# Performance work log

Measured on AMD Instinct MI355X. Metric: run time of the kernel, lower is better.

The kernel has to match this reference:

```python
import jax, jax.numpy as jnp
import numpy as np

HIDDEN = 1024
HEADS = 16
HEAD_DIM = HIDDEN // HEADS


def setup_inputs() -> dict:
    key = jax.random.key(0)
    ks = jax.random.split(key, 7)
    B, S, H = 8, 1024, HIDDEN
    hidden_states = jax.random.normal(ks[0], (B, S, H), dtype=jnp.float32)
    attention_mask = jnp.zeros((B, 1, 1, S), dtype=jnp.float32)
    # Xavier-uniform weights [out, in], zero biases (matches module init)
    limit = float(np.sqrt(6.0 / (H + H)))
    Wq = jax.random.uniform(ks[1], (H, H), minval=-limit, maxval=limit, dtype=jnp.float32)
    Wk = jax.random.uniform(ks[2], (H, H), minval=-limit, maxval=limit, dtype=jnp.float32)
    Wv = jax.random.uniform(ks[3], (H, H), minval=-limit, maxval=limit, dtype=jnp.float32)
    bq = jnp.zeros((H,), dtype=jnp.float32)
    bk = jnp.zeros((H,), dtype=jnp.float32)
    bv = jnp.zeros((H,), dtype=jnp.float32)
    return {"hidden_states": hidden_states, "attention_mask": attention_mask,
            "Wq": Wq, "bq": bq, "Wk": Wk, "bk": bk, "Wv": Wv, "bv": bv}


def _split_heads(x):
    # [B, S, H] -> [B, heads, S, head_dim]
    B, S, _ = x.shape
    return x.reshape(B, S, HEADS, HEAD_DIM).transpose(0, 2, 1, 3)


def reference(hidden_states, attention_mask, Wq, bq, Wk, bk, Wv, bv):
    # Linear projections: y = x @ W^T + b  (weights stored [out, in] as in torch)
    q = _split_heads(hidden_states @ Wq.T + bq)
    k = _split_heads(hidden_states @ Wk.T + bk)
    v = _split_heads(hidden_states @ Wv.T + bv)
    scale = 1.0 / (HEAD_DIM ** 0.5)
    scores = jnp.einsum('bhqd,bhkd->bhqk', q, k) * scale  # [B,heads,S,S]
    scores = scores + attention_mask
    probs = jax.nn.softmax(scores, axis=-1)
    # dropout is identity at inference
    ctx = jnp.einsum('bhqk,bhkd->bhqd', probs, v)
    B, _, S, _ = ctx.shape
    return ctx.transpose(0, 2, 1, 3).reshape(B, S, HIDDEN)
```

## Files before the change

kernel.cpp:

```cpp
#include <hip/hip_runtime.h>
#include <hip/hip_bf16.h>
#include <stdint.h>

#define B_ 8
#define S_ 1024
#define NH_ 16
#define D_ 64
#define H_ 1024
#define M_TOT (B_*S_)
#define LOG2E 1.44269504088896f

typedef __attribute__((ext_vector_type(8))) short short8;
typedef __attribute__((ext_vector_type(4))) float f32x4;
typedef __attribute__((ext_vector_type(16))) float f32x16;

#if __has_builtin(__builtin_amdgcn_exp2f)
#define EXP2(x) __builtin_amdgcn_exp2f(x)
#else
#define EXP2(x) __expf((x) * 0.69314718056f)
#endif

static __device__ __forceinline__ unsigned short f2bf(float f) {
  union { float f; unsigned u; } c; c.f = f;
  unsigned u = c.u;
  return (unsigned short)((u + 0x7fffu + ((u >> 16) & 1u)) >> 16);
}

static __device__ __forceinline__ void gld_lds16(void* lds, const void* g) {
  __builtin_amdgcn_global_load_lds((const __attribute__((address_space(1))) unsigned*)g,
                                   (__attribute__((address_space(3))) unsigned*)lds, 16, 0, 0);
}

#define WAIT_LGKM0() asm volatile("s_waitcnt lgkmcnt(0)" ::: "memory")
#define WAIT_VM(n)   asm volatile("s_waitcnt vmcnt(" #n ")" ::: "memory")
#define SBAR()       __builtin_amdgcn_s_barrier()
#define SCHED0()     __builtin_amdgcn_sched_barrier(0)

__global__ void cvt_f32_bf16(const float* __restrict__ X,
                             const float* __restrict__ Wq,
                             const float* __restrict__ Wk,
                             const float* __restrict__ Wv,
                             unsigned short* __restrict__ Xbf,
                             unsigned short* __restrict__ Wbf) {
  const long long NX = (long long)M_TOT * H_;
  const long long NW = (long long)H_ * H_;
  long long t = (long long)blockIdx.x * blockDim.x + threadIdx.x;
  const long long stride = (long long)gridDim.x * blockDim.x;
  const long long total4 = (NX + 3 * NW) >> 2;
  for (; t < total4; t += stride) {
    long long e = t << 2;
    const float* src; unsigned short* dst;
    if (e < NX) { src = X + e; dst = Xbf + e; }
    else {
      long long r = e - NX;
      int w = (int)(r / NW);
      long long o = r - (long long)w * NW;
      src = (w == 0 ? Wq : (w == 1 ? Wk : Wv)) + o;
      dst = Wbf + (long long)w * NW + o;
    }
    float4 v = *(const float4*)src;
    ushort4 u;
    u.x = f2bf(v.x); u.y = f2bf(v.y); u.z = f2bf(v.z); u.w = f2bf(v.w);
    *(ushort4*)dst = u;
  }
}

#define QBM 256
#define QBN 128
#define QBK 64
#define BUFSZ 49152

__global__ __launch_bounds__(512, 2) void qkv_gemm(
    const unsigned short* __restrict__ Xbf,
    const unsigned short* __restrict__ Wbf,
    const float* __restrict__ bq, const float* __restrict__ bk,
    const float* __restrict__ bv,
    unsigned short* __restrict__ Qo, unsigned short* __restrict__ Ko,
    unsigned short* __restrict__ Vt) {
  __shared__ char lds[3 * BUFSZ];

  const int tid = threadIdx.x;
  const int w = tid >> 6;
  const int l = tid & 63;
  const int lrow = l & 15, lgrp = l >> 4;
  const int wm = w >> 1, wn = w & 1;

  const int orig = blockIdx.x;
  const int id = (orig & 7) * 96 + (orig >> 3);
  const int mtile = (id & 31) * QBM;
  const int rest = id >> 5;
  const int ntile = (rest & 7) * QBN;
  const int z = rest >> 3;

  const unsigned short* Wz = Wbf + (long long)z * H_ * H_;

  const int srow = l >> 3;
  const int sslot = l & 7;
  auto stageA = [&](char* buf, int j, int k0) {
    int row = j * 8 + srow;
    int so = (sslot ^ (row & 7)) * 8;
    gld_lds16(buf + j * 1024, Xbf + (long long)(mtile + row) * H_ + k0 + so);
  };
  auto stageB = [&](char* buf, int j, int k0) {
    int row = j * 8 + srow;
    int so = (sslot ^ (row & 7)) * 8;
    gld_lds16(buf + 32768 + j * 1024, Wz + (long long)(ntile + row) * H_ + k0 + so);
  };

  const int strA = (z == 2 ? wn : wm) * 64;
  const int strB = (z == 2 ? wm : wn) * 64;
  const int offA = (z == 2) ? 32768 : 0;
  const int offB = (z == 2) ? 0 : 32768;
  auto rdA = [&](char* buf, int mh, int sub, int ks) -> short8 {
    int r = strA + mh * 32 + sub * 16 + lrow;
    return *(const short8*)(buf + offA + r * 128 + (((ks * 4 + lgrp) ^ (r & 7)) * 16));
  };
  auto rdB = [&](char* buf, int nh, int sub, int ks) -> short8 {
    int r = strB + nh * 32 + sub * 16 + lrow;
    return *(const short8*)(buf + offB + r * 128 + (((ks * 4 + lgrp) ^ (r & 7)) * 16));
  };

  f32x4 acc[4][4];
  f32x4 zero = {0.f, 0.f, 0.f, 0.f};
  #pragma unroll
  for (int i = 0; i < 4; ++i)
    #pragma unroll
    for (int j = 0; j < 4; ++j) acc[i][j] = zero;

  {
    char* b0p = lds;
    char* b1p = lds + BUFSZ;
    #pragma unroll
    for (int c = 0; c < 4; ++c) stageA(b0p, w * 4 + c, 0);
    stageB(b0p, w * 2 + 0, 0); stageB(b0p, w * 2 + 1, 0);
    #pragma unroll
    for (int c = 0; c < 4; ++c) stageA(b1p, w * 4 + c, QBK);
    stageB(b1p, w * 2 + 0, QBK); stageB(b1p, w * 2 + 1, QBK);
  }
  WAIT_VM(6);
  SBAR();

  #pragma unroll 1
  for (int t = 0; t < 16; ++t) {
    char* buf  = lds + (t % 3) * BUFSZ;
    char* nbuf = lds + ((t + 2) % 3) * BUFSZ;
    const int k0n = (t + 2) * QBK;
    const bool st = (t + 2 < 16);

    short8 af[2][2], b0[2][2], b1[2][2];

    #pragma unroll
    for (int sub = 0; sub < 2; ++sub)
      #pragma unroll
      for (int ks = 0; ks < 2; ++ks) {
        af[sub][ks] = rdA(buf, 0, sub, ks);
        b0[sub][ks] = rdB(buf, 0, sub, ks);
      }
    if (st) { stageA(nbuf, w * 4 + 0, k0n); stageA(nbuf, w * 4 + 1, k0n); }
    SBAR();
    WAIT_LGKM0(); SCHED0();
    __builtin_amdgcn_s_setprio(1);
    #pragma unroll
    for (int sa = 0; sa < 2; ++sa)
      #pragma unroll
      for (int sb = 0; sb < 2; ++sb)
        #pragma unroll
        for (int ks = 0; ks < 2; ++ks)
          acc[sa][sb] = __builtin_amdgcn_mfma_f32_16x16x32_bf16(
              af[sa][ks], b0[sb][ks], acc[sa][sb], 0, 0, 0);
    __builtin_amdgcn_s_setprio(0);
    SBAR();

    #pragma unroll
    for (int sub = 0; sub < 2; ++sub)
      #pragma unroll
      for (int ks = 0; ks < 2; ++ks)
        b1[sub][ks] = rdB(buf, 1, sub, ks);
    if (st) { stageA(nbuf, w * 4 + 2, k0n); stageA(nbuf, w * 4 + 3, k0n); }
    SBAR();
    WAIT_LGKM0(); SCHED0();
    __builtin_amdgcn_s_setprio(1);
    #pragma unroll
    for (int sa = 0; sa < 2; ++sa)
      #pragma unroll
      for (int sb = 0; sb < 2; ++sb)
        #pragma unroll
        for (int ks = 0; ks < 2; ++ks)
          acc[sa][2 + sb] = __builtin_amdgcn_mfma_f32_16x16x32_bf16(
              af[sa][ks], b1[sb][ks], acc[sa][2 + sb], 0, 0, 0);
    __builtin_amdgcn_s_setprio(0);
    SBAR();

    #pragma unroll
    for (int sub = 0; sub < 2; ++sub)
      #pragma unroll
      for (int ks = 0; ks < 2; ++ks)
        af[sub][ks] = rdA(buf, 1, sub, ks);
    if (st) { stageB(nbuf, w * 2 + 0, k0n); stageB(nbuf, w * 2 + 1, k0n); }
    SBAR();
    WAIT_LGKM0(); SCHED0();
    __builtin_amdgcn_s_setprio(1);
    #pragma unroll
    for (int sa = 0; sa < 2; ++sa)
      #pragma unroll
      for (int sb = 0; sb < 2; ++sb)
        #pragma unroll
        for (int ks = 0; ks < 2; ++ks)
          acc[2 + sa][2 + sb] = __builtin_amdgcn_mfma_f32_16x16x32_bf16(
              af[sa][ks], b1[sb][ks], acc[2 + sa][2 + sb], 0, 0, 0);
    __builtin_amdgcn_s_setprio(0);
    SBAR();

    __builtin_amdgcn_s_setprio(1);
    #pragma unroll
    for (int sa = 0; sa < 2; ++sa)
      #pragma unroll
      for (int sb = 0; sb < 2; ++sb)
        #pragma unroll
        for (int ks = 0; ks < 2; ++ks)
          acc[2 + sa][sb] = __builtin_amdgcn_mfma_f32_16x16x32_bf16(
              af[sa][ks], b0[sb][ks], acc[2 + sa][sb], 0, 0, 0);
    __builtin_amdgcn_s_setprio(0);
    if (t < 14) { WAIT_VM(6); } else { WAIT_VM(0); }
    SBAR();
  }

  const float* bias = (z == 0) ? bq : (z == 1) ? bk : bv;
  if (z != 2) {
    unsigned short* O = (z == 0) ? Qo : Ko;
    #pragma unroll
    for (int in = 0; in < 4; ++in) {
      int n = ntile + wn * 64 + in * 16 + lrow;
      float bv_ = bias[n];
      int h = n >> 6, d = n & 63;
      #pragma unroll
      for (int im = 0; im < 4; ++im)
        #pragma unroll
        for (int r = 0; r < 4; ++r) {
          int m = mtile + wm * 64 + im * 16 + lgrp * 4 + r;
          float val = acc[im][in][r] + bv_;
          if (z == 0) val *= 0.125f * LOG2E;
          int b = m >> 10, s = m & 1023;
          O[(((long long)(b * NH_ + h)) * S_ + s) * D_ + d] = f2bf(val);
        }
    }
  } else {
    #pragma unroll
    for (int im = 0; im < 4; ++im)
      #pragma unroll
      for (int r = 0; r < 4; ++r) {
        int nfull = ntile + wn * 64 + im * 16 + lgrp * 4 + r;
        float bv_ = bias[nfull];
        int h = nfull >> 6, d = nfull & 63;
        #pragma unroll
        for (int in = 0; in < 4; ++in) {
          int mfull = mtile + wm * 64 + in * 16 + lrow;
          float val = acc[im][in][r] + bv_;
          int b = mfull >> 10, s = mfull & 1023;
          Vt[(((long long)(b * NH_ + h)) * D_ + d) * S_ + s] = f2bf(val);
        }
      }
  }
}

__global__ __launch_bounds__(256, 2) void attn_fused(
    const unsigned short* __restrict__ Qbf,
    const unsigned short* __restrict__ Kbf,
    const unsigned short* __restrict__ Vtb,
    const float* __restrict__ mask,
    float* __restrict__ out) {
  __shared__ char lds[32768];
  const int tid = threadIdx.x, w = tid >> 6, l = tid & 63;
  const int l31 = l & 31, h = l >> 5;

  const int lid = blockIdx.x;
  const int xcd = lid & 7, k8 = lid >> 3;
  const int bh = xcd * 16 + (k8 >> 2);
  const int qt = k8 & 3;
  const int b = bh >> 4, hd = bh & 15;
  const int q0 = qt * 256 + w * 64;

  const unsigned short* Kg = Kbf + (long long)bh * S_ * D_;
  const unsigned short* Vg = Vtb + (long long)bh * D_ * S_;
  const float* mrow = mask + b * S_;

  {
    const int row = (w * 2) * 8 + (l >> 3);
    const int row1 = (w * 2 + 1) * 8 + (l >> 3);
    const int so = ((l & 7) ^ (row & 7)) * 8;
    const int so1 = ((l & 7) ^ (row1 & 7)) * 8;
    gld_lds16(lds + (w * 2) * 1024,        Kg + (long long)row * D_ + so);
    gld_lds16(lds + (w * 2 + 1) * 1024,    Kg + (long long)row1 * D_ + so1);
    gld_lds16(lds + 8192 + (w * 2) * 1024, Vg + (long long)row * S_ + so);
    gld_lds16(lds + 8192 + (w * 2 + 1) * 1024, Vg + (long long)row1 * S_ + so1);
  }

  short8 qf[2][4];
  #pragma unroll
  for (int qb = 0; qb < 2; ++qb)
    #pragma unroll
    for (int ks = 0; ks < 4; ++ks)
      qf[qb][ks] = *(const short8*)(Qbf + ((long long)bh * S_ + q0 + qb * 32 + l31) * D_ + ks * 16 + 8 * h);

  f32x16 acc[2][2];
  #pragma unroll
  for (int db = 0; db < 2; ++db)
    #pragma unroll
    for (int qb = 0; qb < 2; ++qb)
      #pragma unroll
      for (int r = 0; r < 16; ++r) acc[db][qb][r] = 0.f;
  float m_run[2] = {-1e30f, -1e30f};
  float l_run[2] = {0.f, 0.f};

  __syncthreads();

  for (int kt = 0; kt < S_ / 64; ++kt) {
    const int p = kt & 1;
    char* ldsK = lds + p * 16384;
    char* ldsV = ldsK + 8192;
    const int key0 = kt * 64;

    if (kt < S_ / 64 - 1) {
      char* nb = lds + (p ^ 1) * 16384;
      const int nk0 = key0 + 64;
      #pragma unroll
      for (int t = 0; t < 2; ++t) {
        int j = w * 2 + t;
        int row = j * 8 + (l >> 3);
        int so = ((l & 7) ^ (row & 7)) * 8;
        gld_lds16(nb + j * 1024,        Kg + (long long)(nk0 + row) * D_ + so);
        gld_lds16(nb + 8192 + j * 1024, Vg + (long long)row * S_ + nk0 + so);
      }
    }

    f32x16 sc[2][2];
    #pragma unroll
    for (int kb = 0; kb < 2; ++kb)
      #pragma unroll
      for (int qb = 0; qb < 2; ++qb)
        #pragma unroll
        for (int r = 0; r < 16; ++r) sc[kb][qb][r] = 0.f;

    #pragma unroll
    for (int kb = 0; kb < 2; ++kb) {
      short8 kf[4];
      #pragma unroll
      for (int ks = 0; ks < 4; ++ks) {
        int row = kb * 32 + l31;
        int g = (2 * ks + h) ^ (row & 7);
        kf[ks] = *(const short8*)(ldsK + row * 128 + g * 16);
      }
      __builtin_amdgcn_s_setprio(1);
      #pragma unroll
      for (int qb = 0; qb < 2; ++qb)
        #pragma unroll
        for (int ks = 0; ks < 4; ++ks)
          sc[kb][qb] = __builtin_amdgcn_mfma_f32_32x32x16_bf16(
              kf[ks], qf[qb][ks], sc[kb][qb], 0, 0, 0);
      __builtin_amdgcn_s_setprio(0);
    }

    short8 pfrag[2][4];
    #pragma unroll
    for (int qb = 0; qb < 2; ++qb) {
      float sv[32];
      #pragma unroll
      for (int kb = 0; kb < 2; ++kb)
        #pragma unroll
        for (int rg = 0; rg < 4; ++rg) {
          f32x4 m4 = *(const f32x4*)(mrow + key0 + kb * 32 + rg * 8 + 4 * h);
          #pragma unroll
          for (int c = 0; c < 4; ++c)
            sv[kb * 16 + rg * 4 + c] = fmaf(m4[c], LOG2E, sc[kb][qb][rg * 4 + c]);
        }
      float r16[16];
      #pragma unroll
      for (int i = 0; i < 16; ++i) r16[i] = fmaxf(sv[i], sv[i + 16]);
      #pragma unroll
      for (int i = 0; i < 8; ++i) r16[i] = fmaxf(r16[i], r16[i + 8]);
      #pragma unroll
      for (int i = 0; i < 4; ++i) r16[i] = fmaxf(r16[i], r16[i + 4]);
      float pm = fmaxf(fmaxf(r16[0], r16[1]), fmaxf(r16[2], r16[3]));
      pm = fmaxf(pm, __shfl_xor(pm, 32));
      if (!__all(pm - m_run[qb] <= 11.5f)) {
        float mn = fmaxf(m_run[qb], pm);
        float rs = EXP2(m_run[qb] - mn);
        m_run[qb] = mn;
        l_run[qb] *= rs;
        #pragma unroll
        for (int db = 0; db < 2; ++db)
          #pragma unroll
          for (int r = 0; r < 16; ++r) acc[db][qb][r] *= rs;
      }
      const float mcur = m_run[qb];
      #pragma unroll
      for (int i = 0; i < 32; ++i) sv[i] = EXP2(sv[i] - mcur);
      #pragma unroll
      for (int i = 0; i < 16; ++i) r16[i] = sv[i] + sv[i + 16];
      #pragma unroll
      for (int i = 0; i < 8; ++i) r16[i] = r16[i] + r16[i + 8];
      #pragma unroll
      for (int i = 0; i < 4; ++i) r16[i] = r16[i] + r16[i + 4];
      float ps = (r16[0] + r16[1]) + (r16[2] + r16[3]);
      ps += __shfl_xor(ps, 32);
      l_run[qb] += ps;

      unsigned Wd[8][2];
      #pragma unroll
      for (int j = 0; j < 8; ++j) {
        int base = (j >> 2) * 16 + (j & 3) * 4;
        asm("v_cvt_pk_bf16_f32 %0, %1, %2" : "=v"(Wd[j][0]) : "v"(sv[base + 0]), "v"(sv[base + 1]));
        asm("v_cvt_pk_bf16_f32 %0, %1, %2" : "=v"(Wd[j][1]) : "v"(sv[base + 2]), "v"(sv[base + 3]));
      }
      #pragma unroll
      for (int ks = 0; ks < 4; ++ks) {
        unsigned s0 = h ? Wd[2 * ks][0] : Wd[2 * ks + 1][0];
        unsigned s1 = h ? Wd[2 * ks][1] : Wd[2 * ks + 1][1];
        unsigned r0 = __shfl_xor(s0, 32);
        unsigned r1 = __shfl_xor(s1, 32);
        unsigned o0 = h ? Wd[2 * ks + 1][0] : Wd[2 * ks][0];
        unsigned o1 = h ? Wd[2 * ks + 1][1] : Wd[2 * ks][1];
        union { unsigned u[4]; short8 s; } fu;
        fu.u[0] = h ? r0 : o0;
        fu.u[1] = h ? r1 : o1;
        fu.u[2] = h ? o0 : r0;
        fu.u[3] = h ? o1 : r1;
        pfrag[qb][ks] = fu.s;
      }
    }

    #pragma unroll
    for (int db = 0; db < 2; ++db) {
      short8 vf[4];
      #pragma unroll
      for (int ks = 0; ks < 4; ++ks) {
        int row = db * 32 + l31;
        int g = (2 * ks + h) ^ (row & 7);
        vf[ks] = *(const short8*)(ldsV + row * 128 + g * 16);
      }
      __builtin_amdgcn_s_setprio(1);
      #pragma unroll
      for (int qb = 0; qb < 2; ++qb)
        #pragma unroll
        for (int ks = 0; ks < 4; ++ks)
          acc[db][qb] = __builtin_amdgcn_mfma_f32_32x32x16_bf16(
              vf[ks], pfrag[qb][ks], acc[db][qb], 0, 0, 0);
      __builtin_amdgcn_s_setprio(0);
    }

    __syncthreads();
  }

  #pragma unroll
  for (int qb = 0; qb < 2; ++qb) {
    float inv = 1.0f / l_run[qb];
    int q = q0 + qb * 32 + l31;
    float* orow = out + ((long long)b * S_ + q) * H_ + hd * D_;
    #pragma unroll
    for (int db = 0; db < 2; ++db)
      #pragma unroll
      for (int rg = 0; rg < 4; ++rg) {
        f32x4 v4;
        #pragma unroll
        for (int c = 0; c < 4; ++c) v4[c] = acc[db][qb][rg * 4 + c] * inv;
        *(f32x4*)(orow + db * 32 + rg * 8 + 4 * h) = v4;
      }
  }
}

extern "C" void kernel_launch(void* const* d_in, const int* in_sizes, int n_in,
                              void* d_out, int out_size, void* d_ws, size_t ws_size,
                              hipStream_t stream) {
  const float* X    = (const float*)d_in[0];
  const float* mask = (const float*)d_in[1];
  const float* Wq   = (const float*)d_in[2];
  const float* bq   = (const float*)d_in[3];
  const float* Wk   = (const float*)d_in[4];
  const float* bk   = (const float*)d_in[5];
  const float* Wv   = (const float*)d_in[6];
  const float* bv   = (const float*)d_in[7];
  float* out = (float*)d_out;

  char* ws = (char*)d_ws;
  unsigned short* Xbf = (unsigned short*)ws;
  unsigned short* Wbf = (unsigned short*)(ws + 16777216);
  unsigned short* Qb  = (unsigned short*)(ws + 23068672);
  unsigned short* Kb  = (unsigned short*)(ws + 39845888);
  unsigned short* Vt  = (unsigned short*)(ws + 56623104);

  hipLaunchKernelGGL(cvt_f32_bf16, dim3(2048), dim3(256), 0, stream,
                     X, Wq, Wk, Wv, Xbf, Wbf);
  hipLaunchKernelGGL(qkv_gemm, dim3(768), dim3(512), 0, stream,
                     Xbf, Wbf, bq, bk, bv, Qb, Kb, Vt);
  hipLaunchKernelGGL(attn_fused, dim3(512), dim3(256), 0, stream,
                     Qb, Kb, Vt, mask, out);
}
```

Baseline: 146.0 us.

## Reshape QKV GEMM tile to 128x256 with per-XCD M-tile grouping

Changes the QKV projection block tile from 256x128 to 128x256, puts the 8 waves in a 2x4 arrangement, and restructures the inner loop from four MFMA phases into two, with all A fragments loaded once per k-step. Block-to-tile mapping now gives each XCD a contiguous range of M tiles that covers every N tile of that range, aiming for better L2 reuse of the activation rows. The epilogue still uses wm*64/wn*64 indexing, which may not match the new 2x4 wave layout for the z==2 transposed path or for the output coverage. Register pressure rises from holding eight A fragments.

After: 132.6 us. -9.2%, faster.

```diff
diff --git a/kernel.cpp b/kernel.cpp
--- a/kernel.cpp
+++ b/kernel.cpp
@@ -65,8 +65,8 @@
   }
 }
 
-#define QBM 256
-#define QBN 128
+#define QBM 128
+#define QBN 256
 #define QBK 64
 #define BUFSZ 49152
 
@@ -83,14 +83,15 @@
   const int w = tid >> 6;
   const int l = tid & 63;
   const int lrow = l & 15, lgrp = l >> 4;
-  const int wm = w >> 1, wn = w & 1;
+  const int wm = w >> 2, wn = w & 3;
 
   const int orig = blockIdx.x;
-  const int id = (orig & 7) * 96 + (orig >> 3);
-  const int mtile = (id & 31) * QBM;
-  const int rest = id >> 5;
-  const int ntile = (rest & 7) * QBN;
-  const int z = rest >> 3;
+  const int xcd = orig & 7;
+  const int slot = orig >> 3;
+  const int z = slot >> 5;
+  const int i = slot & 31;
+  const int mtile = (xcd * 8 + (i >> 2)) * QBM;
+  const int ntile = (i & 3) * QBN;
 
   const unsigned short* Wz = Wbf + (long long)z * H_ * H_;
 
@@ -104,38 +105,38 @@
   auto stageB = [&](char* buf, int j, int k0) {
     int row = j * 8 + srow;
     int so = (sslot ^ (row & 7)) * 8;
-    gld_lds16(buf + 32768 + j * 1024, Wz + (long long)(ntile + row) * H_ + k0 + so);
+    gld_lds16(buf + 16384 + j * 1024, Wz + (long long)(ntile + row) * H_ + k0 + so);
   };
 
   const int strA = (z == 2 ? wn : wm) * 64;
   const int strB = (z == 2 ? wm : wn) * 64;
-  const int offA = (z == 2) ? 32768 : 0;
-  const int offB = (z == 2) ? 0 : 32768;
-  auto rdA = [&](char* buf, int mh, int sub, int ks) -> short8 {
-    int r = strA + mh * 32 + sub * 16 + lrow;
+  const int offA = (z == 2) ? 16384 : 0;
+  const int offB = (z == 2) ? 0 : 16384;
+  auto rdA = [&](char* buf, int fi, int ks) -> short8 {
+    int r = strA + fi * 16 + lrow;
     return *(const short8*)(buf + offA + r * 128 + (((ks * 4 + lgrp) ^ (r & 7)) * 16));
   };
-  auto rdB = [&](char* buf, int nh, int sub, int ks) -> short8 {
-    int r = strB + nh * 32 + sub * 16 + lrow;
+  auto rdB = [&](char* buf, int fi, int ks) -> short8 {
+    int r = strB + fi * 16 + lrow;
     return *(const short8*)(buf + offB + r * 128 + (((ks * 4 + lgrp) ^ (r & 7)) * 16));
   };
 
   f32x4 acc[4][4];
   f32x4 zero = {0.f, 0.f, 0.f, 0.f};
   #pragma unroll
-  for (int i = 0; i < 4; ++i)
-    #pragma unroll
-    for (int j = 0; j < 4; ++j) acc[i][j] = zero;
+  for (int a = 0; a < 4; ++a)
+    #pragma unroll
+    for (int c = 0; c < 4; ++c) acc[a][c] = zero;
 
   {
     char* b0p = lds;
     char* b1p = lds + BUFSZ;
-    #pragma unroll
-    for (int c = 0; c < 4; ++c) stageA(b0p, w * 4 + c, 0);
-    stageB(b0p, w * 2 + 0, 0); stageB(b0p, w * 2 + 1, 0);
-    #pragma unroll
-    for (int c = 0; c < 4; ++c) stageA(b1p, w * 4 + c, QBK);
-    stageB(b1p, w * 2 + 0, QBK); stageB(b1p, w * 2 + 1, QBK);
+    stageA(b0p, 2 * w + 0, 0); stageA(b0p, 2 * w + 1, 0);
+    #pragma unroll
+    for (int c = 0; c < 4; ++c) stageB(b0p, 4 * w + c, 0);
+    stageA(b1p, 2 * w + 0, QBK); stageA(b1p, 2 * w + 1, QBK);
+    #pragma unroll
+    for (int c = 0; c < 4; ++c) stageB(b1p, 4 * w + c, QBK);
   }
   WAIT_VM(6);
   SBAR();
@@ -147,79 +148,49 @@
     const int k0n = (t + 2) * QBK;
     const bool st = (t + 2 < 16);
 
-    short8 af[2][2], b0[2][2], b1[2][2];
-
-    #pragma unroll
-    for (int sub = 0; sub < 2; ++sub)
-      #pragma unroll
-      for (int ks = 0; ks < 2; ++ks) {
-        af[sub][ks] = rdA(buf, 0, sub, ks);
-        b0[sub][ks] = rdB(buf, 0, sub, ks);
-      }
-    if (st) { stageA(nbuf, w * 4 + 0, k0n); stageA(nbuf, w * 4 + 1, k0n); }
+    short8 af[4][2], bf[2][2];
+
+    #pragma unroll
+    for (int fi = 0; fi < 4; ++fi)
+      #pragma unroll
+      for (int ks = 0; ks < 2; ++ks) af[fi][ks] = rdA(buf, fi, ks);
+    #pragma unroll
+    for (int fi = 0; fi < 2; ++fi)
+      #pragma unroll
+      for (int ks = 0; ks < 2; ++ks) bf[fi][ks] = rdB(buf, fi, ks);
+    if (st) { stageA(nbuf, 2 * w + 0, k0n); stageA(nbuf, 2 * w + 1, k0n);
+              stageB(nbuf, 4 * w + 0, k0n); }
     SBAR();
     WAIT_LGKM0(); SCHED0();
     __builtin_amdgcn_s_setprio(1);
     #pragma unroll
-    for (int sa = 0; sa < 2; ++sa)
-      #pragma unroll
-      for (int sb = 0; sb < 2; ++sb)
+    for (int im = 0; im < 4; ++im)
+      #pragma unroll
+      for (int in = 0; in < 2; ++in)
         #pragma unroll
         for (int ks = 0; ks < 2; ++ks)
-          acc[sa][sb] = __builtin_amdgcn_mfma_f32_16x16x32_bf16(
-              af[sa][ks], b0[sb][ks], acc[sa][sb], 0, 0, 0);
+          acc[im][in] = __builtin_amdgcn_mfma_f32_16x16x32_bf16(
+              af[im][ks], bf[in][ks], acc[im][in], 0, 0, 0);
     __builtin_amdgcn_s_setprio(0);
     SBAR();
 
     #pragma unroll
-    for (int sub = 0; sub < 2; ++sub)
-      #pragma unroll
-      for (int ks = 0; ks < 2; ++ks)
-        b1[sub][ks] = rdB(buf, 1, sub, ks);
-    if (st) { stageA(nbuf, w * 4 + 2, k0n); stageA(nbuf, w * 4 + 3, k0n); }
+    for (int fi = 0; fi < 2; ++fi)
+      #pragma unroll
+      for (int ks = 0; ks < 2; ++ks) bf[fi][ks] = rdB(buf, 2 + fi, ks);
+    if (st) { stageB(nbuf, 4 * w + 1, k0n); stageB(nbuf, 4 * w + 2, k0n);
+              stageB(nbuf, 4 * w + 3, k0n); }
     SBAR();
     WAIT_LGKM0(); SCHED0();
     __builtin_amdgcn_s_setprio(1);
     #pragma unroll
-    for (int sa = 0; sa < 2; ++sa)
-      #pragma unroll
-      for (int sb = 0; sb < 2; ++sb)
+    for (int im = 0; im < 4; ++im)
+      #pragma unroll
+      for (int in = 0; in < 2; ++in)
         #pragma unroll
         for (int ks = 0; ks < 2; ++ks)
-          acc[sa][2 + sb] = __builtin_amdgcn_mfma_f32_16x16x32_bf16(
-              af[sa][ks], b1[sb][ks], acc[sa][2 + sb], 0, 0, 0);
-    __builtin_amdgcn_s_setprio(0);
-    SBAR();
-
-    #pragma unroll
-    for (int sub = 0; sub < 2; ++sub)
-      #pragma unroll
-      for (int ks = 0; ks < 2; ++ks)
-        af[sub][ks] = rdA(buf, 1, sub, ks);
-    if (st) { stageB(nbuf, w * 2 + 0, k0n); stageB(nbuf, w * 2 + 1, k0n); }
-    SBAR();
-    WAIT_LGKM0(); SCHED0();
-    __builtin_amdgcn_s_setprio(1);
-    #pragma unroll
-    for (int sa = 0; sa < 2; ++sa)
-      #pragma unroll
-      for (int sb = 0; sb < 2; ++sb)
-        #pragma unroll
-        for (int ks = 0; ks < 2; ++ks)
-          acc[2 + sa][2 + sb] = __builtin_amdgcn_mfma_f32_16x16x32_bf16(
-              af[sa][ks], b1[sb][ks], acc[2 + sa][2 + sb], 0, 0, 0);
-    __builtin_amdgcn_s_setprio(0);
-    SBAR();
-
-    __builtin_amdgcn_s_setprio(1);
-    #pragma unroll
-    for (int sa = 0; sa < 2; ++sa)
-      #pragma unroll
-      for (int sb = 0; sb < 2; ++sb)
-        #pragma unroll
-        for (int ks = 0; ks < 2; ++ks)
-          acc[2 + sa][sb] = __builtin_amdgcn_mfma_f32_16x16x32_bf16(
-              af[sa][ks], b0[sb][ks], acc[2 + sa][sb], 0, 0, 0);
+          acc[im][2 + in] = __builtin_amdgcn_mfma_f32_16x16x32_bf16(
+              af[im][ks], bf[in][ks], acc[im][2 + in], 0, 0, 0);
     __builtin_amdgcn_s_setprio(0);
     if (t < 14) { WAIT_VM(6); } else { WAIT_VM(0); }
     SBAR();
```
